# Kernel tuning notes

Hardware: AMD Instinct MI355X
Metric: run time of the kernel (lower is better)

## Reference

```python
import jax, jax.numpy as jnp
import numpy as np

N = 50000   # nodes
E = 1000000 # edges
D_IN = 64
D_OUT = 64
R = 16      # relations (num_rels == num_bases)


def setup_inputs() -> dict:
    key = jax.random.key(0)
    k1, k2, k3, k4, k5, k6, k7 = jax.random.split(key, 7)
    node_features = jax.random.normal(k1, (N, D_IN), dtype=jnp.float32)
    edge_src = jax.random.randint(k2, (E,), 0, N, dtype=jnp.int32)
    edge_dst = jax.random.randint(k3, (E,), 0, N, dtype=jnp.int32)
    edge_type = jax.random.randint(k4, (E,), 0, R, dtype=jnp.int32)
    edge_norm = jax.random.uniform(k5, (E,), dtype=jnp.float32)
    weight = jax.random.normal(k6, (R, D_IN, D_OUT), dtype=jnp.float32) * 0.1
    bias = jax.random.normal(k7, (D_OUT,), dtype=jnp.float32) * 0.1
    return {
        "node_features": node_features,
        "edge_src": edge_src,
        "edge_dst": edge_dst,
        "edge_type": edge_type,
        "edge_norm": edge_norm,
        "weight": weight,
        "bias": bias,
    }


def reference(node_features, edge_src, edge_dst, edge_type, edge_norm, weight, bias):
    # gather source features and per-edge relation weight matrices
    h_src = node_features[edge_src]              # [E, D_IN]
    w = weight[edge_type]                        # [E, D_IN, D_OUT]
    # per-edge bmm: [E,1,D_IN] @ [E,D_IN,D_OUT] -> [E,D_OUT]
    msg = jnp.einsum('ed,edo->eo', h_src, w)
    msg = msg * edge_norm[:, None]               # norm scaling
    # scatter-sum aggregation over destination nodes
    node_repr = jax.ops.segment_sum(msg, edge_dst, num_segments=N)  # [N, D_OUT]
    node_repr = node_repr + bias
    return jax.nn.relu(node_repr)
```

## Files before the change

### kernel.cpp

```cpp
#include <hip/hip_runtime.h>
#include <hip/hip_bf16.h>


#define NN 50000
#define EE 1000000
#define RR 16
#define NBLK 256
#define EPB 3907
#define BSH 6
#define NBUK 782
#define NS (NBUK * NBLK)
#define SCAP 2048

typedef __attribute__((ext_vector_type(8))) short short8;
typedef __attribute__((ext_vector_type(4))) float f32x4;

static __device__ inline unsigned short f2bf(float f) {
  union { __hip_bfloat16 h; unsigned short u; } cv;
  cv.h = __float2bfloat16(f);
  return cv.u;
}
static __device__ inline float bf2f(unsigned short u) {
  union { unsigned i; float f; } cv;
  cv.i = ((unsigned)u) << 16;
  return cv.f;
}

__global__ __launch_bounds__(256) void k_wthist(const float* __restrict__ W,
                                                const int* __restrict__ edst,
                                                unsigned short* __restrict__ Wt,
                                                int* __restrict__ cntT) {
  __shared__ __align__(16) char smem[64 * 72 * 2];
  const int bid = blockIdx.x, tid = threadIdx.x;
  if (bid < RR) {
    auto Wl = reinterpret_cast<unsigned short(*)[72]>(smem);
    const int r = bid;
    for (int i = tid; i < 4096; i += 256) Wl[i & 63][i >> 6] = f2bf(W[(r << 12) + i]);
    __syncthreads();
    const int o = tid >> 2, kc = (tid & 3) << 4;
    const short8 v0 = *reinterpret_cast<const short8*>(&Wl[o][kc]);
    const short8 v1 = *reinterpret_cast<const short8*>(&Wl[o][kc + 8]);
    unsigned short* dst = Wt + (r << 12) + (o << 6) + kc;
    *reinterpret_cast<short8*>(dst) = v0;
    *reinterpret_cast<short8*>(dst + 8) = v1;
    return;
  }
  int* cnt = reinterpret_cast<int*>(smem);
  const int bl = bid - RR;
  for (int i = tid; i < NBUK; i += 256) cnt[i] = 0;
  __syncthreads();
  const int e0 = bl * EPB, e1 = min(EE, e0 + EPB);
  for (int e = e0 + tid; e < e1; e += 256) atomicAdd(&cnt[edst[e] >> BSH], 1);
  __syncthreads();
  for (int i = tid; i < NBUK; i += 256) cntT[i * NBLK + bl] = cnt[i];
}

__global__ __launch_bounds__(256) void k_gemm(const float* __restrict__ nf,
                                              const unsigned short* __restrict__ Wt,
                                              unsigned short* __restrict__ X) {
  __shared__ __align__(16) unsigned short Wl[4][64][72];
  const int tid = threadIdx.x;
  const int lane = tid & 63, wv = tid >> 6;
  const int lr = lane & 15, lg = lane >> 4;
  const int node = (blockIdx.x << 6) + (wv << 4) + lr;
  const int r0 = blockIdx.y << 2;
  #pragma unroll
  for (int rr = 0; rr < 4; ++rr) {
    const unsigned short* src = Wt + (((size_t)(r0 + rr)) << 12) + (tid << 4);
    const short8 v0 = *reinterpret_cast<const short8*>(src);
    const short8 v1 = *reinterpret_cast<const short8*>(src + 8);
    unsigned short* dst = &Wl[rr][tid >> 2][(tid & 3) << 4];
    *reinterpret_cast<short8*>(dst) = v0;
    *reinterpret_cast<short8*>(dst + 8) = v1;
  }
  short8 bf0, bf1;
  if (node < NN) {
    const float* ap = nf + (size_t)node * 64 + lg * 8;
    float4 v0 = *reinterpret_cast<const float4*>(ap);
    float4 v1 = *reinterpret_cast<const float4*>(ap + 4);
    float4 v2 = *reinterpret_cast<const float4*>(ap + 32);
    float4 v3 = *reinterpret_cast<const float4*>(ap + 36);
    bf0 = short8{(short)f2bf(v0.x), (short)f2bf(v0.y), (short)f2bf(v0.z), (short)f2bf(v0.w),
                 (short)f2bf(v1.x), (short)f2bf(v1.y), (short)f2bf(v1.z), (short)f2bf(v1.w)};
    bf1 = short8{(short)f2bf(v2.x), (short)f2bf(v2.y), (short)f2bf(v2.z), (short)f2bf(v2.w),
                 (short)f2bf(v3.x), (short)f2bf(v3.y), (short)f2bf(v3.z), (short)f2bf(v3.w)};
  } else {
    bf0 = short8{0, 0, 0, 0, 0, 0, 0, 0};
    bf1 = bf0;
  }
  __syncthreads();
  #pragma unroll
  for (int rr = 0; rr < 4; ++rr) {
    const int r = r0 + rr;
    short8 a[8];
    #pragma unroll
    for (int c = 0; c < 4; ++c) {
      a[2 * c] = *reinterpret_cast<const short8*>(&Wl[rr][(c << 4) + lr][lg << 3]);
      a[2 * c + 1] = *reinterpret_cast<const short8*>(&Wl[rr][(c << 4) + lr][32 + (lg << 3)]);
    }
    f32x4 acc[4];
    #pragma unroll
    for (int c = 0; c < 4; ++c) {
      acc[c] = f32x4{0.f, 0.f, 0.f, 0.f};
      acc[c] = __builtin_amdgcn_mfma_f32_16x16x32_bf16(a[2 * c], bf0, acc[c], 0, 0, 0);
      acc[c] = __builtin_amdgcn_mfma_f32_16x16x32_bf16(a[2 * c + 1], bf1, acc[c], 0, 0, 0);
    }
    if (node < NN) {
      #pragma unroll
      for (int c = 0; c < 4; ++c) {
        uint2 p;
        p.x = (unsigned)f2bf(acc[c][0]) | ((unsigned)f2bf(acc[c][1]) << 16);
        p.y = (unsigned)f2bf(acc[c][2]) | ((unsigned)f2bf(acc[c][3]) << 16);
        *reinterpret_cast<uint2*>(&X[((size_t)r * NN + node) * 64 + (c << 4) + (lg << 2)]) = p;
      }
    }
  }
}

__global__ __launch_bounds__(256) void k_scan_a(const int* __restrict__ cntT,
                                                int* __restrict__ offsT,
                                                int* __restrict__ bsum) {
  __shared__ int s[256];
  const int t = threadIdx.x;
  const int i = blockIdx.x * 256 + t;
  const int v = cntT[i];
  s[t] = v;
  __syncthreads();
  #pragma unroll
  for (int off = 1; off < 256; off <<= 1) {
    const int x = (t >= off) ? s[t - off] : 0;
    __syncthreads();
    s[t] += x;
    __syncthreads();
  }
  offsT[i] = s[t] - v;
  if (t == 255) bsum[blockIdx.x] = s[255];
}

__global__ __launch_bounds__(1024) void k_scan_b(const int* __restrict__ bsum,
                                                 int* __restrict__ bsum2) {
  __shared__ int s[1024];
  const int t = threadIdx.x;
  const int v = (t < NBUK) ? bsum[t] : 0;
  s[t] = v;
  __syncthreads();
  #pragma unroll
  for (int off = 1; off < 1024; off <<= 1) {
    const int x = (t >= off) ? s[t - off] : 0;
    __syncthreads();
    s[t] += x;
    __syncthreads();
  }
  if (t < NBUK) bsum2[t] = s[t] - v;
  if (t == NBUK) bsum2[NBUK] = EE;
}

__global__ __launch_bounds__(256) void k_scatter(const int* __restrict__ esrc,
                                                 const int* __restrict__ edst,
                                                 const int* __restrict__ etyp,
                                                 const float* __restrict__ enorm,
                                                 const int* __restrict__ offsT,
                                                 const int* __restrict__ bsum2,
                                                 uint2* __restrict__ rec) {
  __shared__ int cur[NBUK];
  const int bl = blockIdx.x, tid = threadIdx.x;
  for (int i = tid; i < NBUK; i += 256) cur[i] = offsT[i * NBLK + bl] + bsum2[i];
  __syncthreads();
  const int e0 = bl * EPB, e1 = min(EE, e0 + EPB);
  for (int e = e0 + tid; e < e1; e += 256) {
    const int d = edst[e];
    const int pos = atomicAdd(&cur[d >> BSH], 1);
    rec[pos] = make_uint2(((unsigned)(etyp[e] * NN + esrc[e]) << 6) | (unsigned)(d & 63),
                          __float_as_uint(enorm[e]));
  }
}

__global__ __launch_bounds__(256) void k_nsort(const int* __restrict__ bsum2,
                                               uint2* __restrict__ rec,
                                               int* __restrict__ noffs) {
  __shared__ uint2 sbuf[SCAP];
  __shared__ int cnt[64], cur[64];
  const int bu = blockIdx.x, tid = threadIdx.x;
  const int s = bsum2[bu];
  const int e = bsum2[bu + 1];
  const int n = e - s;
  if (tid < 64) cnt[tid] = 0;
  __syncthreads();
  if (n > SCAP) {
    if (tid < 64) noffs[(bu << BSH) + tid] = -1;
    return;
  }
  for (int i = tid; i < n; i += 256) {
    const uint2 r = rec[s + i];
    sbuf[i] = r;
    atomicAdd(&cnt[r.x & 63u], 1);
  }
  __syncthreads();
  if (tid < 64) {
    const int v = cnt[tid];
    int x = v;
    #pragma unroll
    for (int off = 1; off < 64; off <<= 1) {
      const int t = __shfl_up(x, off, 64);
      if (tid >= off) x += t;
    }
    cur[tid] = x - v;
    noffs[(bu << BSH) + tid] = s + x - v;
  }
  __syncthreads();
  for (int i = tid; i < n; i += 256) {
    const uint2 r = sbuf[i];
    const int pos = atomicAdd(&cur[r.x & 63u], 1);
    rec[s + pos] = r;
  }
}

__global__ __launch_bounds__(256) void k_ngather(const uint2* __restrict__ rec,
                                                 const int* __restrict__ noffs,
                                                 const int* __restrict__ bsum2,
                                                 const unsigned short* __restrict__ X,
                                                 const float* __restrict__ bias,
                                                 float* __restrict__ out) {
  const int w = (int)((blockIdx.x * 256 + threadIdx.x) >> 6);
  const int lane = threadIdx.x & 63;
  if (w >= NN) return;
  const int quarter = lane >> 4, d4 = lane & 15;
  const int bu = w >> BSH;
  float4 acc = {0.f, 0.f, 0.f, 0.f};
  const int jb = noffs[w];
  if (jb >= 0) {
    const int je = ((w & 63) == 63) ? bsum2[bu + 1] : noffs[w + 1];
    for (int base = jb; base < je; base += 64) {
      const int deg = min(64, je - base);
      unsigned rxs = 0;
      float rns = 0.f;
      if (lane < deg) {
        const uint2 r = rec[base + lane];
        rxs = r.x >> 6;
        rns = __uint_as_float(r.y);
      }
      int u = 0;
      for (; u + 16 <= deg; u += 16) {
        unsigned row[4];
        float nm[4];
        uint2 xv[4];
        #pragma unroll
        for (int k = 0; k < 4; ++k) {
          const int i = u + 4 * k + quarter;
          row[k] = (unsigned)__shfl((int)rxs, i, 64);
          nm[k] = __shfl(rns, i, 64);
        }
        #pragma unroll
        for (int k = 0; k < 4; ++k)
          xv[k] = *reinterpret_cast<const uint2*>(X + (size_t)row[k] * 64 + (d4 << 2));
        #pragma unroll
        for (int k = 0; k < 4; ++k) {
          acc.x = fmaf(nm[k], bf2f((unsigned short)(xv[k].x & 0xffffu)), acc.x);
          acc.y = fmaf(nm[k], bf2f((unsigned short)(xv[k].x >> 16)), acc.y);
          acc.z = fmaf(nm[k], bf2f((unsigned short)(xv[k].y & 0xffffu)), acc.z);
          acc.w = fmaf(nm[k], bf2f((unsigned short)(xv[k].y >> 16)), acc.w);
        }
      }
      for (; u + 8 <= deg; u += 8) {
        const int i0 = u + quarter, i1 = u + 4 + quarter;
        const unsigned row0 = (unsigned)__shfl((int)rxs, i0, 64);
        const float n0 = __shfl(rns, i0, 64);
        const unsigned row1 = (unsigned)__shfl((int)rxs, i1, 64);
        const float n1 = __shfl(rns, i1, 64);
        const uint2 x0 = *reinterpret_cast<const uint2*>(X + (size_t)row0 * 64 + (d4 << 2));
        const uint2 x1 = *reinterpret_cast<const uint2*>(X + (size_t)row1 * 64 + (d4 << 2));
        acc.x = fmaf(n0, bf2f((unsigned short)(x0.x & 0xffffu)), acc.x);
        acc.y = fmaf(n0, bf2f((unsigned short)(x0.x >> 16)), acc.y);
        acc.z = fmaf(n0, bf2f((unsigned short)(x0.y & 0xffffu)), acc.z);
        acc.w = fmaf(n0, bf2f((unsigned short)(x0.y >> 16)), acc.w);
        acc.x = fmaf(n1, bf2f((unsigned short)(x1.x & 0xffffu)), acc.x);
        acc.y = fmaf(n1, bf2f((unsigned short)(x1.x >> 16)), acc.y);
        acc.z = fmaf(n1, bf2f((unsigned short)(x1.y & 0xffffu)), acc.z);
        acc.w = fmaf(n1, bf2f((unsigned short)(x1.y >> 16)), acc.w);
      }
      for (; u < deg; u += 4) {
        const int i = u + quarter;
        const int ic = min(i, deg - 1);
        const unsigned row = (unsigned)__shfl((int)rxs, ic, 64);
        float n = __shfl(rns, ic, 64);
        n = (i < deg) ? n : 0.f;
        const uint2 x = *reinterpret_cast<const uint2*>(X + (size_t)row * 64 + (d4 << 2));
        acc.x = fmaf(n, bf2f((unsigned short)(x.x & 0xffffu)), acc.x);
        acc.y = fmaf(n, bf2f((unsigned short)(x.x >> 16)), acc.y);
        acc.z = fmaf(n, bf2f((unsigned short)(x.y & 0xffffu)), acc.z);
        acc.w = fmaf(n, bf2f((unsigned short)(x.y >> 16)), acc.w);
      }
    }
  } else {
    if (quarter == 0) {
      const int s = bsum2[bu];
      const int e = bsum2[bu + 1];
      const unsigned dl = (unsigned)(w & 63);
      for (int j = s; j < e; ++j) {
        const uint2 r = rec[j];
        if ((r.x & 63u) == dl) {
          const float n = __uint_as_float(r.y);
          const uint2 x =
              *reinterpret_cast<const uint2*>(X + (size_t)(r.x >> 6) * 64 + (d4 << 2));
          acc.x = fmaf(n, bf2f((unsigned short)(x.x & 0xffffu)), acc.x);
          acc.y = fmaf(n, bf2f((unsigned short)(x.x >> 16)), acc.y);
          acc.z = fmaf(n, bf2f((unsigned short)(x.y & 0xffffu)), acc.z);
          acc.w = fmaf(n, bf2f((unsigned short)(x.y >> 16)), acc.w);
        }
      }
    }
  }
  acc.x += __shfl_xor(acc.x, 16, 64);
  acc.y += __shfl_xor(acc.y, 16, 64);
  acc.z += __shfl_xor(acc.z, 16, 64);
  acc.w += __shfl_xor(acc.w, 16, 64);
  acc.x += __shfl_xor(acc.x, 32, 64);
  acc.y += __shfl_xor(acc.y, 32, 64);
  acc.z += __shfl_xor(acc.z, 32, 64);
  acc.w += __shfl_xor(acc.w, 32, 64);
  if (quarter == 0) {
    const float4 b = reinterpret_cast<const float4*>(bias)[d4];
    float4 o;
    o.x = fmaxf(acc.x + b.x, 0.f);
    o.y = fmaxf(acc.y + b.y, 0.f);
    o.z = fmaxf(acc.z + b.z, 0.f);
    o.w = fmaxf(acc.w + b.w, 0.f);
    reinterpret_cast<float4*>(out)[(size_t)w * 16 + d4] = o;
  }
}

extern "C" void kernel_launch(void* const* d_in, const int* in_sizes, int n_in,
                              void* d_out, int out_size, void* d_ws, size_t ws_size,
                              hipStream_t stream) {
  const float* nf = (const float*)d_in[0];
  const int* esrc = (const int*)d_in[1];
  const int* edst = (const int*)d_in[2];
  const int* etyp = (const int*)d_in[3];
  const float* enorm = (const float*)d_in[4];
  const float* W = (const float*)d_in[5];
  const float* bias = (const float*)d_in[6];
  float* out = (float*)d_out;

  char* ws = (char*)d_ws;
  unsigned short* X = (unsigned short*)ws;
  unsigned short* Wt = (unsigned short*)(ws + 102400000);
  uint2* rec = (uint2*)(ws + 102531072);
  int* cntT = (int*)(ws + 110531072);
  int* offsT = (int*)(ws + 111331840);
  int* bsum = (int*)(ws + 112132608);
  int* bsum2 = (int*)(ws + 112135736);
  int* noffs = (int*)(ws + 112138868);

  k_wthist<<<RR + NBLK, 256, 0, stream>>>(W, edst, Wt, cntT);
  dim3 g1(NBUK, 4);
  k_gemm<<<g1, 256, 0, stream>>>(nf, Wt, X);
  k_scan_a<<<NS / 256, 256, 0, stream>>>(cntT, offsT, bsum);
  k_scan_b<<<1, 1024, 0, stream>>>(bsum, bsum2);
  k_scatter<<<NBLK, 256, 0, stream>>>(esrc, edst, etyp, enorm, offsT, bsum2, rec);
  k_nsort<<<NBUK, 256, 0, stream>>>(bsum2, rec, noffs);
  k_ngather<<<(NN * 64 + 255) / 256, 256, 0, stream>>>(rec, noffs, bsum2, X, bias, out);
}
```

Measured before the change: 104.1 us.

## Replace two-level bucket scan with global atomic bucket counts and in-scatter scan

Each histogram block now reserves its per-bucket offset with a global atomicAdd on bucket totals instead of writing a block-by-bucket count matrix. The scatter kernel computes the exclusive scan of the 782 bucket totals itself and adds the per-block offsets, so the two separate scan kernels are removed. This drops two kernel launches and the full count-matrix scan, at the cost of a memset plus global atomic contention. Edge order within a bucket becomes nondeterministic, which can slightly change float summation order.

```diff
diff --git a/kernel.cpp b/kernel.cpp
--- a/kernel.cpp
+++ b/kernel.cpp
@@ -9,7 +9,6 @@
 #define EPB 3907
 #define BSH 6
 #define NBUK 782
-#define NS (NBUK * NBLK)
 #define SCAP 2048
 
 typedef __attribute__((ext_vector_type(8))) short short8;
@@ -29,7 +28,8 @@
 __global__ __launch_bounds__(256) void k_wthist(const float* __restrict__ W,
                                                 const int* __restrict__ edst,
                                                 unsigned short* __restrict__ Wt,
-                                                int* __restrict__ cntT) {
+                                                int* __restrict__ gcnt,
+                                                int* __restrict__ blkoff) {
   __shared__ __align__(16) char smem[64 * 72 * 2];
   const int bid = blockIdx.x, tid = threadIdx.x;
   if (bid < RR) {
@@ -52,7 +52,10 @@
   const int e0 = bl * EPB, e1 = min(EE, e0 + EPB);
   for (int e = e0 + tid; e < e1; e += 256) atomicAdd(&cnt[edst[e] >> BSH], 1);
   __syncthreads();
-  for (int i = tid; i < NBUK; i += 256) cntT[i * NBLK + bl] = cnt[i];
+  for (int i = tid; i < NBUK; i += 256) {
+    const int c = cnt[i];
+    blkoff[i * NBLK + bl] = c ? atomicAdd(&gcnt[i], c) : 0;
+  }
 }
 
 __global__ __launch_bounds__(256) void k_gemm(const float* __restrict__ nf,
@@ -117,14 +120,28 @@
   }
 }
 
-__global__ __launch_bounds__(256) void k_scan_a(const int* __restrict__ cntT,
-                                                int* __restrict__ offsT,
-                                                int* __restrict__ bsum) {
+__global__ __launch_bounds__(256) void k_scatter(const int* __restrict__ esrc,
+                                                 const int* __restrict__ edst,
+                                                 const int* __restrict__ etyp,
+                                                 const float* __restrict__ enorm,
+                                                 const int* __restrict__ gcnt,
+                                                 const int* __restrict__ blkoff,
+                                                 int* __restrict__ bsum2,
+                                                 uint2* __restrict__ rec) {
+  __shared__ int bloc[NBUK];
   __shared__ int s[256];
-  const int t = threadIdx.x;
-  const int i = blockIdx.x * 256 + t;
-  const int v = cntT[i];
-  s[t] = v;
+  __shared__ int cur[NBUK];
+  const int bl = blockIdx.x, t = threadIdx.x;
+  int v[4];
+  int tot = 0;
+  const int b4 = t << 2;
+  #pragma unroll
+  for (int k = 0; k < 4; ++k) {
+    const int idx = b4 + k;
+    v[k] = (idx < NBUK) ? gcnt[idx] : 0;
+    tot += v[k];
+  }
+  s[t] = tot;
   __syncthreads();
   #pragma unroll
   for (int off = 1; off < 256; off <<= 1) {
@@ -133,41 +150,22 @@
     s[t] += x;
     __syncthreads();
   }
-  offsT[i] = s[t] - v;
-  if (t == 255) bsum[blockIdx.x] = s[255];
-}
-
-__global__ __launch_bounds__(1024) void k_scan_b(const int* __restrict__ bsum,
-                                                 int* __restrict__ bsum2) {
-  __shared__ int s[1024];
-  const int t = threadIdx.x;
-  const int v = (t < NBUK) ? bsum[t] : 0;
-  s[t] = v;
-  __syncthreads();
-  #pragma unroll
-  for (int off = 1; off < 1024; off <<= 1) {
-    const int x = (t >= off) ? s[t - off] : 0;
-    __syncthreads();
-    s[t] += x;
-    __syncthreads();
-  }
-  if (t < NBUK) bsum2[t] = s[t] - v;
-  if (t == NBUK) bsum2[NBUK] = EE;
-}
-
-__global__ __launch_bounds__(256) void k_scatter(const int* __restrict__ esrc,
-                                                 const int* __restrict__ edst,
-                                                 const int* __restrict__ etyp,
-                                                 const float* __restrict__ enorm,
-                                                 const int* __restrict__ offsT,
-                                                 const int* __restrict__ bsum2,
-                                                 uint2* __restrict__ rec) {
-  __shared__ int cur[NBUK];
-  const int bl = blockIdx.x, tid = threadIdx.x;
-  for (int i = tid; i < NBUK; i += 256) cur[i] = offsT[i * NBLK + bl] + bsum2[i];
+  int run = s[t] - tot;
+  #pragma unroll
+  for (int k = 0; k < 4; ++k) {
+    const int idx = b4 + k;
+    if (idx < NBUK) bloc[idx] = run;
+    run += v[k];
+  }
+  __syncthreads();
+  if (bl == 0) {
+    for (int i = t; i < NBUK; i += 256) bsum2[i] = bloc[i];
+    if (t == 0) bsum2[NBUK] = EE;
+  }
+  for (int i = t; i < NBUK; i += 256) cur[i] = bloc[i] + blkoff[i * NBLK + bl];
   __syncthreads();
   const int e0 = bl * EPB, e1 = min(EE, e0 + EPB);
-  for (int e = e0 + tid; e < e1; e += 256) {
+  for (int e = e0 + t; e < e1; e += 256) {
     const int d = edst[e];
     const int pos = atomicAdd(&cur[d >> BSH], 1);
     rec[pos] = make_uint2(((unsigned)(etyp[e] * NN + esrc[e]) << 6) | (unsigned)(d & 63),
@@ -345,18 +343,16 @@
   unsigned short* X = (unsigned short*)ws;
   unsigned short* Wt = (unsigned short*)(ws + 102400000);
   uint2* rec = (uint2*)(ws + 102531072);
-  int* cntT = (int*)(ws + 110531072);
-  int* offsT = (int*)(ws + 111331840);
-  int* bsum = (int*)(ws + 112132608);
-  int* bsum2 = (int*)(ws + 112135736);
-  int* noffs = (int*)(ws + 112138868);
-
-  k_wthist<<<RR + NBLK, 256, 0, stream>>>(W, edst, Wt, cntT);
+  int* blkoff = (int*)(ws + 110531072);
+  int* gcnt = (int*)(ws + 111331840);
+  int* bsum2 = (int*)(ws + 111334968);
+  int* noffs = (int*)(ws + 111338100);
+
+  hipMemsetAsync(gcnt, 0, NBUK * 4, stream);
+  k_wthist<<<RR + NBLK, 256, 0, stream>>>(W, edst, Wt, gcnt, blkoff);
   dim3 g1(NBUK, 4);
   k_gemm<<<g1, 256, 0, stream>>>(nf, Wt, X);
-  k_scan_a<<<NS / 256, 256, 0, stream>>>(cntT, offsT, bsum);
-  k_scan_b<<<1, 1024, 0, stream>>>(bsum, bsum2);
-  k_scatter<<<NBLK, 256, 0, stream>>>(esrc, edst, etyp, enorm, offsT, bsum2, rec);
+  k_scatter<<<NBLK, 256, 0, stream>>>(esrc, edst, etyp, enorm, gcnt, blkoff, bsum2, rec);
   k_nsort<<<NBUK, 256, 0, stream>>>(bsum2, rec, noffs);
   k_ngather<<<(NN * 64 + 255) / 256, 256, 0, stream>>>(rec, noffs, bsum2, X, bias, out);
 }
```

Measured after the change: 112.1 us. 1.08x slower.
